# Performance work log

Measured on AMD Instinct MI355X. Metric: run time of the kernel, lower is better.

The kernel has to match this reference:

```python
import jax, jax.numpy as jnp
import numpy as np

N, E, C_IN, HID, G, L = 100000, 1600000, 64, 32, 128, 3
NEG_SLOPE = 0.01  # F.leaky_relu default


def setup_inputs() -> dict:
    key = jax.random.key(0)
    ks = jax.random.split(key, 10)
    x = jax.random.normal(ks[0], (N, C_IN), dtype=jnp.float32)
    src = jax.random.randint(ks[1], (E,), 0, N, dtype=jnp.int32)
    dst = jax.random.randint(ks[2], (E,), 0, N, dtype=jnp.int32)
    batch = jnp.sort(jax.random.randint(ks[3], (N,), 0, G, dtype=jnp.int32))
    def glorot(k, fan_in, fan_out):
        lim = np.sqrt(6.0 / (fan_in + fan_out)).astype(np.float32)
        return jax.random.uniform(k, (fan_in, fan_out), jnp.float32, -lim, lim)
    W0 = glorot(ks[4], C_IN, HID); b0 = jnp.zeros((HID,), jnp.float32)
    W1 = glorot(ks[5], HID, HID);  b1 = jnp.zeros((HID,), jnp.float32)
    W2 = glorot(ks[6], HID, HID);  b2 = jnp.zeros((HID,), jnp.float32)
    return {"x": x, "W0": W0, "b0": b0, "W1": W1, "b1": b1,
            "W2": W2, "b2": b2, "src": src, "dst": dst, "batch": batch}


def _gcn_conv(x, W, b, src, dst, dinv):
    # PyG GCNConv: h = x W; aggregate with sym-norm (A + I)
    h = x @ W                                   # [N, H]
    coef = (dinv[src] * dinv[dst])[:, None]     # [E, 1]
    msg = h[src] * coef                         # gather + scale
    agg = jax.ops.segment_sum(msg, dst, num_segments=N)
    agg = agg + h * (dinv * dinv)[:, None]      # self-loop term
    return agg + b


def _mean_pool(x, batch, counts):
    s = jax.ops.segment_sum(x, batch, num_segments=G)
    return s / counts[:, None]


def reference(x, W0, b0, W1, b1, W2, b2, src, dst, batch):
    # degree with self loops (edge weight 1), as PyG gcn_norm does
    deg = jax.ops.segment_sum(jnp.ones((E,), x.dtype), dst, num_segments=N) + 1.0
    dinv = jax.lax.rsqrt(deg)
    counts = jnp.maximum(
        jax.ops.segment_sum(jnp.ones((N,), x.dtype), batch, num_segments=G), 1.0)
    params = [(W0, b0), (W1, b1), (W2, b2)]
    feats = []
    h = x
    for W, b in params:
        h = _gcn_conv(h, W, b, src, dst, dinv)
        h = jax.nn.leaky_relu(h, NEG_SLOPE)
        feats.append(_mean_pool(h, batch, counts))
    merge = jnp.mean(jnp.stack(feats, axis=0), axis=0)  # [G, HID]
    return merge
```

## Files before the change

kernel.cpp:

```cpp
#include <hip/hip_runtime.h>
#include <hip/hip_bf16.h>

#define NN 100000
#define NE 1600000
#define CIN 64
#define HIDN 32
#define NG 128
#define SLOPE 0.01f
#define NBLK 98
#define SCAT_BLOCKS 782
#define MM0_BLOCKS 12500
#define AGG_BLOCKS 3125


__global__ __launch_bounds__(256) void k_rank(const int* __restrict__ dst,
                                              int* __restrict__ deg,
                                              unsigned int* __restrict__ rank) {
  int i = blockIdx.x * 256 + threadIdx.x;
  if (i * 8 >= NE) return;
  int4 a = ((const int4*)dst)[2 * i];
  int4 b = ((const int4*)dst)[2 * i + 1];
  unsigned int r0 = atomicAdd(&deg[a.x], 1);
  unsigned int r1 = atomicAdd(&deg[a.y], 1);
  unsigned int r2 = atomicAdd(&deg[a.z], 1);
  unsigned int r3 = atomicAdd(&deg[a.w], 1);
  unsigned int r4 = atomicAdd(&deg[b.x], 1);
  unsigned int r5 = atomicAdd(&deg[b.y], 1);
  unsigned int r6 = atomicAdd(&deg[b.z], 1);
  unsigned int r7 = atomicAdd(&deg[b.w], 1);
  uint2 packed;
  packed.x = r0 | (r1 << 8) | (r2 << 16) | (r3 << 24);
  packed.y = r4 | (r5 << 8) | (r6 << 16) | (r7 << 24);
  ((uint2*)rank)[i] = packed;
}


__global__ __launch_bounds__(256) void k_scan1(const int* __restrict__ deg,
                                               int* __restrict__ bsum,
                                               float* __restrict__ dinv,
                                               const int* __restrict__ batch,
                                               float* __restrict__ cinv,
                                               float* __restrict__ out) {
  __shared__ int s[256];
  __shared__ int sb[NG + 1];
  int t = threadIdx.x;
  int base = blockIdx.x * 1024 + t * 4;
  int sum = 0;
#pragma unroll
  for (int j = 0; j < 4; ++j) {
    int idx = base + j;
    if (idx < NN) {
      int d = deg[idx];
      sum += d;
      dinv[idx] = rsqrtf((float)d + 1.0f);
    }
  }
  s[t] = sum;
  __syncthreads();
  for (int o = 128; o > 0; o >>= 1) {
    if (t < o) s[t] += s[t + o];
    __syncthreads();
  }
  if (t == 0) bsum[blockIdx.x] = s[0];
  if (blockIdx.x == 0) {
    if (t <= NG) {
      int lo = 0, hi = NN;
      while (lo < hi) {
        int mid = (lo + hi) >> 1;
        if (batch[mid] < t) lo = mid + 1; else hi = mid;
      }
      sb[t] = lo;
    }
    for (int i = t; i < NG * HIDN; i += 256) out[i] = 0.f;
    __syncthreads();
    if (t < NG) {
      int c = sb[t + 1] - sb[t];
      cinv[t] = 1.0f / (3.0f * fmaxf((float)c, 1.0f));
    }
  }
}


__global__ __launch_bounds__(256) void k_scan3(const int* __restrict__ deg,
                                               const int* __restrict__ bsum,
                                               int* __restrict__ rowp) {
  __shared__ int s[256];
  __shared__ int sb2[128];
  int t = threadIdx.x;
  if (t < 128) sb2[t] = (t < NBLK) ? bsum[t] : 0;
  int base = blockIdx.x * 1024 + t * 4;
  int d0 = 0, d1 = 0, d2 = 0, d3 = 0;
  if (base < NN) d0 = deg[base];
  if (base + 1 < NN) d1 = deg[base + 1];
  if (base + 2 < NN) d2 = deg[base + 2];
  if (base + 3 < NN) d3 = deg[base + 3];
  int ts = d0 + d1 + d2 + d3;
  s[t] = ts;
  __syncthreads();
  for (int o = 1; o < 128; o <<= 1) {
    int v = (t < 128 && t >= o) ? sb2[t - o] : 0;
    __syncthreads();
    if (t < 128) sb2[t] += v;
    __syncthreads();
  }
  for (int o = 1; o < 256; o <<= 1) {
    int v = (t >= o) ? s[t - o] : 0;
    __syncthreads();
    s[t] += v;
    __syncthreads();
  }
  int blockoff = blockIdx.x ? sb2[blockIdx.x - 1] : 0;
  int run = blockoff + s[t] - ts;
  if (base < NN) { rowp[base] = run; run += d0; }
  if (base + 1 < NN) { rowp[base + 1] = run; run += d1; }
  if (base + 2 < NN) { rowp[base + 2] = run; run += d2; }
  if (base + 3 < NN) { rowp[base + 3] = run; run += d3; }
  if (blockIdx.x == NBLK - 1 && t == 255) rowp[NN] = run;
}


__global__ __launch_bounds__(256) void k_sm(const int* __restrict__ src,
                                            const int* __restrict__ dst,
                                            const unsigned int* __restrict__ rank,
                                            const int* __restrict__ rowp,
                                            int* __restrict__ col,
                                            const float* __restrict__ x,
                                            const float* __restrict__ W0,
                                            const float* __restrict__ dinv,
                                            __hip_bfloat16* __restrict__ hs) {
  __shared__ float sW[CIN * HIDN];
  if (blockIdx.x < SCAT_BLOCKS) {
    int i = blockIdx.x * 256 + threadIdx.x;
    if (i * 8 >= NE) return;
    int4 da = ((const int4*)dst)[2 * i];
    int4 db = ((const int4*)dst)[2 * i + 1];
    uint2 rr = ((const uint2*)rank)[i];
    int4 sa = ((const int4*)src)[2 * i];
    int4 sb = ((const int4*)src)[2 * i + 1];
    col[rowp[da.x] + (int)(rr.x & 0xff)] = sa.x;
    col[rowp[da.y] + (int)((rr.x >> 8) & 0xff)] = sa.y;
    col[rowp[da.z] + (int)((rr.x >> 16) & 0xff)] = sa.z;
    col[rowp[da.w] + (int)(rr.x >> 24)] = sa.w;
    col[rowp[db.x] + (int)(rr.y & 0xff)] = sb.x;
    col[rowp[db.y] + (int)((rr.y >> 8) & 0xff)] = sb.y;
    col[rowp[db.z] + (int)((rr.y >> 16) & 0xff)] = sb.z;
    col[rowp[db.w] + (int)(rr.y >> 24)] = sb.w;
    return;
  }
  int t = threadIdx.x;
  for (int i = t; i < CIN * HIDN; i += 256) sW[i] = W0[i];
  __syncthreads();
  int gid = (blockIdx.x - SCAT_BLOCKS) * 256 + t;
  int node = gid >> 5;
  int f = gid & 31;
  const float* xr = x + node * CIN;
  float acc = 0.f;
#pragma unroll
  for (int k = 0; k < CIN; ++k) acc += xr[k] * sW[k * HIDN + f];
  hs[node * HIDN + f] = __float2bfloat16(acc * dinv[node]);
}


template <int FUSE>
__global__ __launch_bounds__(256) void k_agg(const __hip_bfloat16* __restrict__ hs,
                                             const int* __restrict__ rowp,
                                             const int* __restrict__ col,
                                             const float* __restrict__ dinv,
                                             const int* __restrict__ batch,
                                             const float* __restrict__ cinv,
                                             const float* __restrict__ bias,
                                             const float* __restrict__ Wn,
                                             __hip_bfloat16* __restrict__ hs_next,
                                             float* __restrict__ pool) {
  __shared__ float vrow[32][32];
  __shared__ float sWn[FUSE ? HIDN * HIDN : 1];
  const int t = threadIdx.x;
  const int f = t & 31;
  const int sub = t >> 5;
  const int base = blockIdx.x * 32;

  if (FUSE) {
#pragma unroll
    for (int i = 0; i < 4; ++i) sWn[t + i * 256] = Wn[t + i * 256];
  }

  const float bf = bias[f];
  float pacc = 0.f;
  int gcur = -1;
#pragma unroll
  for (int it = 0; it < 4; ++it) {
    const int i = base + it * 8 + sub;
    float acc = __bfloat162float(hs[i * HIDN + f]);
    const int rs = rowp[i];
    const int re = rowp[i + 1];
    int e = rs;
    for (; e + 8 <= re; e += 8) {
      const int c0 = __builtin_nontemporal_load(col + e);
      const int c1 = __builtin_nontemporal_load(col + e + 1);
      const int c2 = __builtin_nontemporal_load(col + e + 2);
      const int c3 = __builtin_nontemporal_load(col + e + 3);
      const int c4 = __builtin_nontemporal_load(col + e + 4);
      const int c5 = __builtin_nontemporal_load(col + e + 5);
      const int c6 = __builtin_nontemporal_load(col + e + 6);
      const int c7 = __builtin_nontemporal_load(col + e + 7);
      const float v0 = __bfloat162float(hs[c0 * HIDN + f]);
      const float v1 = __bfloat162float(hs[c1 * HIDN + f]);
      const float v2 = __bfloat162float(hs[c2 * HIDN + f]);
      const float v3 = __bfloat162float(hs[c3 * HIDN + f]);
      const float v4 = __bfloat162float(hs[c4 * HIDN + f]);
      const float v5 = __bfloat162float(hs[c5 * HIDN + f]);
      const float v6 = __bfloat162float(hs[c6 * HIDN + f]);
      const float v7 = __bfloat162float(hs[c7 * HIDN + f]);
      acc += ((v0 + v1) + (v2 + v3)) + ((v4 + v5) + (v6 + v7));
    }
    for (; e + 4 <= re; e += 4) {
      const int c0 = __builtin_nontemporal_load(col + e);
      const int c1 = __builtin_nontemporal_load(col + e + 1);
      const int c2 = __builtin_nontemporal_load(col + e + 2);
      const int c3 = __builtin_nontemporal_load(col + e + 3);
      const float v0 = __bfloat162float(hs[c0 * HIDN + f]);
      const float v1 = __bfloat162float(hs[c1 * HIDN + f]);
      const float v2 = __bfloat162float(hs[c2 * HIDN + f]);
      const float v3 = __bfloat162float(hs[c3 * HIDN + f]);
      acc += (v0 + v1) + (v2 + v3);
    }
    for (; e < re; ++e) acc += __bfloat162float(hs[col[e] * HIDN + f]);
    float v = acc * dinv[i] + bf;
    v = v > 0.f ? v : SLOPE * v;
    if (FUSE) vrow[it * 8 + sub][f] = v;
    const int g = batch[i];
    if (g != gcur) {
      if (gcur >= 0) unsafeAtomicAdd(&pool[gcur * HIDN + f], pacc * cinv[gcur]);
      gcur = g;
      pacc = 0.f;
    }
    pacc += v;
  }
  if (gcur >= 0) unsafeAtomicAdd(&pool[gcur * HIDN + f], pacc * cinv[gcur]);

  if (FUSE) {
    __syncthreads();
#pragma unroll
    for (int q = 0; q < 4; ++q) {
      const int li = sub * 4 + q;
      const int i = base + li;
      float a = 0.f;
#pragma unroll
      for (int k = 0; k < HIDN; ++k) a += vrow[li][k] * sWn[k * HIDN + f];
      hs_next[i * HIDN + f] = __float2bfloat16(a * dinv[i]);
    }
  }
}


extern "C" void kernel_launch(void* const* d_in, const int* in_sizes, int n_in,
                              void* d_out, int out_size, void* d_ws, size_t ws_size,
                              hipStream_t stream) {
  const float* x = (const float*)d_in[0];
  const float* W0 = (const float*)d_in[1];
  const float* b0 = (const float*)d_in[2];
  const float* W1 = (const float*)d_in[3];
  const float* b1 = (const float*)d_in[4];
  const float* W2 = (const float*)d_in[5];
  const float* b2 = (const float*)d_in[6];
  const int* src = (const int*)d_in[7];
  const int* dst = (const int*)d_in[8];
  const int* batch = (const int*)d_in[9];
  float* out = (float*)d_out;

  char* ws = (char*)d_ws;
  auto carve = [&](size_t bytes) -> char* {
    char* p = ws;
    ws += (bytes + 255) & ~(size_t)255;
    return p;
  };
  int* deg = (int*)carve(NN * 4);
  unsigned int* rank = (unsigned int*)carve((size_t)NE);
  int* rowp = (int*)carve((NN + 1) * 4);
  int* bsum = (int*)carve(128 * 4);
  float* dinv = (float*)carve(NN * 4);
  float* cinv = (float*)carve(NG * 4);
  int* col = (int*)carve((size_t)NE * 4);
  __hip_bfloat16* hsA = (__hip_bfloat16*)carve((size_t)NN * HIDN * 2);
  __hip_bfloat16* hsB = (__hip_bfloat16*)carve((size_t)NN * HIDN * 2);

  hipMemsetAsync(deg, 0, NN * 4, stream);

  k_rank<<<SCAT_BLOCKS, 256, 0, stream>>>(dst, deg, rank);
  k_scan1<<<NBLK, 256, 0, stream>>>(deg, bsum, dinv, batch, cinv, out);
  k_scan3<<<NBLK, 256, 0, stream>>>(deg, bsum, rowp);
  k_sm<<<SCAT_BLOCKS + MM0_BLOCKS, 256, 0, stream>>>(src, dst, rank, rowp, col,
                                                     x, W0, dinv, hsA);
  k_agg<1><<<AGG_BLOCKS, 256, 0, stream>>>(hsA, rowp, col, dinv, batch, cinv,
                                           b0, W1, hsB, out);
  k_agg<1><<<AGG_BLOCKS, 256, 0, stream>>>(hsB, rowp, col, dinv, batch, cinv,
                                           b1, W2, hsA, out);
  k_agg<0><<<AGG_BLOCKS, 256, 0, stream>>>(hsA, rowp, col, dinv, batch, cinv,
                                           b2, nullptr, nullptr, out);
}
```

Baseline: 415.7 us.

## Fuse two-pass degree scan into single-pass decoupled look-back scan; prefetch CSR columns

Replaces the two-kernel prefix scan (block sums, then a rescan with offsets) with one kernel that uses decoupled look-back flags, so each block publishes its aggregate and inclusive prefix and spins on its predecessors. This removes one kernel launch and one reread of the degree array, and the flags are zeroed by the same memset that clears the degree array. Separately, the aggregation inner loop now software-pipelines the column-index loads, fetching the next 8 indices while gathering the current 8 feature values. The look-back relies on all 98 blocks being resident at once, and the pipelined loop uses more registers.

```diff
diff --git a/kernel.cpp b/kernel.cpp
--- a/kernel.cpp
+++ b/kernel.cpp
@@ -11,6 +11,7 @@
 #define SCAT_BLOCKS 782
 #define MM0_BLOCKS 12500
 #define AGG_BLOCKS 3125
+#define SCAN_RDY 0x40000000u
 
 
 __global__ __launch_bounds__(256) void k_rank(const int* __restrict__ dst,
@@ -35,34 +36,61 @@
 }
 
 
-__global__ __launch_bounds__(256) void k_scan1(const int* __restrict__ deg,
-                                               int* __restrict__ bsum,
-                                               float* __restrict__ dinv,
-                                               const int* __restrict__ batch,
-                                               float* __restrict__ cinv,
-                                               float* __restrict__ out) {
+__global__ __launch_bounds__(256) void k_scan(const int* __restrict__ deg,
+                                              int* __restrict__ rowp,
+                                              float* __restrict__ dinv,
+                                              const int* __restrict__ batch,
+                                              float* __restrict__ cinv,
+                                              float* __restrict__ out,
+                                              unsigned int* __restrict__ flagA,
+                                              unsigned int* __restrict__ flagP) {
   __shared__ int s[256];
+  __shared__ int sboff;
   __shared__ int sb[NG + 1];
-  int t = threadIdx.x;
-  int base = blockIdx.x * 1024 + t * 4;
-  int sum = 0;
-#pragma unroll
-  for (int j = 0; j < 4; ++j) {
-    int idx = base + j;
-    if (idx < NN) {
-      int d = deg[idx];
-      sum += d;
-      dinv[idx] = rsqrtf((float)d + 1.0f);
-    }
-  }
-  s[t] = sum;
+  const int t = threadIdx.x;
+  const int b = blockIdx.x;
+  const int base = b * 1024 + t * 4;
+  int d0 = 0, d1 = 0, d2 = 0, d3 = 0;
+  if (base < NN) { d0 = deg[base]; dinv[base] = rsqrtf((float)d0 + 1.0f); }
+  if (base + 1 < NN) { d1 = deg[base + 1]; dinv[base + 1] = rsqrtf((float)d1 + 1.0f); }
+  if (base + 2 < NN) { d2 = deg[base + 2]; dinv[base + 2] = rsqrtf((float)d2 + 1.0f); }
+  if (base + 3 < NN) { d3 = deg[base + 3]; dinv[base + 3] = rsqrtf((float)d3 + 1.0f); }
+  const int ts = d0 + d1 + d2 + d3;
+  s[t] = ts;
   __syncthreads();
-  for (int o = 128; o > 0; o >>= 1) {
-    if (t < o) s[t] += s[t + o];
+  for (int o = 1; o < 256; o <<= 1) {
+    int v = (t >= o) ? s[t - o] : 0;
     __syncthreads();
-  }
-  if (t == 0) bsum[blockIdx.x] = s[0];
-  if (blockIdx.x == 0) {
+    s[t] += v;
+    __syncthreads();
+  }
+  const int total = s[255];
+  if (t == 0) {
+    __threadfence();
+    atomicExch(&flagA[b], (unsigned)total | SCAN_RDY);
+    unsigned run = 0;
+    if (b > 0) {
+      int j = b - 1;
+      while (j >= 0) {
+        unsigned p = atomicAdd(&flagP[j], 0u);
+        if (p & SCAN_RDY) { run += p & 0x3FFFFFFFu; break; }
+        unsigned a = atomicAdd(&flagA[j], 0u);
+        if (a & SCAN_RDY) { run += a & 0x3FFFFFFFu; --j; }
+      }
+    }
+    __threadfence();
+    atomicExch(&flagP[b], (run + (unsigned)total) | SCAN_RDY);
+    sboff = (int)run;
+  }
+  __syncthreads();
+  int run = sboff + s[t] - ts;
+  if (base < NN) { rowp[base] = run; run += d0; }
+  if (base + 1 < NN) { rowp[base + 1] = run; run += d1; }
+  if (base + 2 < NN) { rowp[base + 2] = run; run += d2; }
+  if (base + 3 < NN) { rowp[base + 3] = run; run += d3; }
+  if (b == NBLK - 1 && t == 255) rowp[NN] = run;
+
+  if (b == 0) {
     if (t <= NG) {
       int lo = 0, hi = NN;
       while (lo < hi) {
@@ -78,44 +106,6 @@
       cinv[t] = 1.0f / (3.0f * fmaxf((float)c, 1.0f));
     }
   }
-}
-
-
-__global__ __launch_bounds__(256) void k_scan3(const int* __restrict__ deg,
-                                               const int* __restrict__ bsum,
-                                               int* __restrict__ rowp) {
-  __shared__ int s[256];
-  __shared__ int sb2[128];
-  int t = threadIdx.x;
-  if (t < 128) sb2[t] = (t < NBLK) ? bsum[t] : 0;
-  int base = blockIdx.x * 1024 + t * 4;
-  int d0 = 0, d1 = 0, d2 = 0, d3 = 0;
-  if (base < NN) d0 = deg[base];
-  if (base + 1 < NN) d1 = deg[base + 1];
-  if (base + 2 < NN) d2 = deg[base + 2];
-  if (base + 3 < NN) d3 = deg[base + 3];
-  int ts = d0 + d1 + d2 + d3;
-  s[t] = ts;
-  __syncthreads();
-  for (int o = 1; o < 128; o <<= 1) {
-    int v = (t < 128 && t >= o) ? sb2[t - o] : 0;
-    __syncthreads();
-    if (t < 128) sb2[t] += v;
-    __syncthreads();
-  }
-  for (int o = 1; o < 256; o <<= 1) {
-    int v = (t >= o) ? s[t - o] : 0;
-    __syncthreads();
-    s[t] += v;
-    __syncthreads();
-  }
-  int blockoff = blockIdx.x ? sb2[blockIdx.x - 1] : 0;
-  int run = blockoff + s[t] - ts;
-  if (base < NN) { rowp[base] = run; run += d0; }
-  if (base + 1 < NN) { rowp[base + 1] = run; run += d1; }
-  if (base + 2 < NN) { rowp[base + 2] = run; run += d2; }
-  if (base + 3 < NN) { rowp[base + 3] = run; run += d3; }
-  if (blockIdx.x == NBLK - 1 && t == 255) rowp[NN] = run;
 }
 
 
@@ -194,15 +184,37 @@
     const int rs = rowp[i];
     const int re = rowp[i + 1];
     int e = rs;
-    for (; e + 8 <= re; e += 8) {
-      const int c0 = __builtin_nontemporal_load(col + e);
-      const int c1 = __builtin_nontemporal_load(col + e + 1);
-      const int c2 = __builtin_nontemporal_load(col + e + 2);
-      const int c3 = __builtin_nontemporal_load(col + e + 3);
-      const int c4 = __builtin_nontemporal_load(col + e + 4);
-      const int c5 = __builtin_nontemporal_load(col + e + 5);
-      const int c6 = __builtin_nontemporal_load(col + e + 6);
-      const int c7 = __builtin_nontemporal_load(col + e + 7);
+    const int nfull = (re - rs) >> 3;
+    if (nfull > 0) {
+      int c0 = __builtin_nontemporal_load(col + e);
+      int c1 = __builtin_nontemporal_load(col + e + 1);
+      int c2 = __builtin_nontemporal_load(col + e + 2);
+      int c3 = __builtin_nontemporal_load(col + e + 3);
+      int c4 = __builtin_nontemporal_load(col + e + 4);
+      int c5 = __builtin_nontemporal_load(col + e + 5);
+      int c6 = __builtin_nontemporal_load(col + e + 6);
+      int c7 = __builtin_nontemporal_load(col + e + 7);
+      for (int bi = 1; bi < nfull; ++bi) {
+        const int n0 = __builtin_nontemporal_load(col + e + 8);
+        const int n1 = __builtin_nontemporal_load(col + e + 9);
+        const int n2 = __builtin_nontemporal_load(col + e + 10);
+        const int n3 = __builtin_nontemporal_load(col + e + 11);
+        const int n4 = __builtin_nontemporal_load(col + e + 12);
+        const int n5 = __builtin_nontemporal_load(col + e + 13);
+        const int n6 = __builtin_nontemporal_load(col + e + 14);
+        const int n7 = __builtin_nontemporal_load(col + e + 15);
+        const float v0 = __bfloat162float(hs[c0 * HIDN + f]);
+        const float v1 = __bfloat162float(hs[c1 * HIDN + f]);
+        const float v2 = __bfloat162float(hs[c2 * HIDN + f]);
+        const float v3 = __bfloat162float(hs[c3 * HIDN + f]);
+        const float v4 = __bfloat162float(hs[c4 * HIDN + f]);
+        const float v5 = __bfloat162float(hs[c5 * HIDN + f]);
+        const float v6 = __bfloat162float(hs[c6 * HIDN + f]);
+        const float v7 = __bfloat162float(hs[c7 * HIDN + f]);
+        acc += ((v0 + v1) + (v2 + v3)) + ((v4 + v5) + (v6 + v7));
+        c0 = n0; c1 = n1; c2 = n2; c3 = n3; c4 = n4; c5 = n5; c6 = n6; c7 = n7;
+        e += 8;
+      }
       const float v0 = __bfloat162float(hs[c0 * HIDN + f]);
       const float v1 = __bfloat162float(hs[c1 * HIDN + f]);
       const float v2 = __bfloat162float(hs[c2 * HIDN + f]);
@@ -212,8 +224,9 @@
       const float v6 = __bfloat162float(hs[c6 * HIDN + f]);
       const float v7 = __bfloat162float(hs[c7 * HIDN + f]);
       acc += ((v0 + v1) + (v2 + v3)) + ((v4 + v5) + (v6 + v7));
-    }
-    for (; e + 4 <= re; e += 4) {
+      e += 8;
+    }
+    if (re - e >= 4) {
       const int c0 = __builtin_nontemporal_load(col + e);
       const int c1 = __builtin_nontemporal_load(col + e + 1);
       const int c2 = __builtin_nontemporal_load(col + e + 2);
@@ -223,6 +236,7 @@
       const float v2 = __bfloat162float(hs[c2 * HIDN + f]);
       const float v3 = __bfloat162float(hs[c3 * HIDN + f]);
       acc += (v0 + v1) + (v2 + v3);
+      e += 4;
     }
     for (; e < re; ++e) acc += __bfloat162float(hs[col[e] * HIDN + f]);
     float v = acc * dinv[i] + bf;
@@ -274,21 +288,21 @@
     ws += (bytes + 255) & ~(size_t)255;
     return p;
   };
+  unsigned int* flagA = (unsigned int*)carve(512);
+  unsigned int* flagP = (unsigned int*)carve(512);
   int* deg = (int*)carve(NN * 4);
   unsigned int* rank = (unsigned int*)carve((size_t)NE);
   int* rowp = (int*)carve((NN + 1) * 4);
-  int* bsum = (int*)carve(128 * 4);
   float* dinv = (float*)carve(NN * 4);
   float* cinv = (float*)carve(NG * 4);
   int* col = (int*)carve((size_t)NE * 4);
   __hip_bfloat16* hsA = (__hip_bfloat16*)carve((size_t)NN * HIDN * 2);
   __hip_bfloat16* hsB = (__hip_bfloat16*)carve((size_t)NN * HIDN * 2);
 
-  hipMemsetAsync(deg, 0, NN * 4, stream);
+  hipMemsetAsync(flagA, 0, 1024 + ((NN * 4 + 255) & ~255), stream);
 
   k_rank<<<SCAT_BLOCKS, 256, 0, stream>>>(dst, deg, rank);
-  k_scan1<<<NBLK, 256, 0, stream>>>(deg, bsum, dinv, batch, cinv, out);
-  k_scan3<<<NBLK, 256, 0, stream>>>(deg, bsum, rowp);
+  k_scan<<<NBLK, 256, 0, stream>>>(deg, rowp, dinv, batch, cinv, out, flagA, flagP);
   k_sm<<<SCAT_BLOCKS + MM0_BLOCKS, 256, 0, stream>>>(src, dst, rank, rowp, col,
                                                      x, W0, dinv, hsA);
   k_agg<1><<<AGG_BLOCKS, 256, 0, stream>>>(hsA, rowp, col, dinv, batch, cinv,
```

After: 414.2 us. No clear change (-0.4%).
